# Kernel optimization log

Hardware: AMD Instinct MI355X
Metric: run time of the kernel (lower is better)

## Reference

```python
import jax, jax.numpy as jnp
import numpy as np

EMBED_DIM = 1024
NUM_HEADS = 16
HEAD_DIM = EMBED_DIM // NUM_HEADS


def setup_inputs() -> dict:
    key = jax.random.key(0)
    ks = jax.random.split(key, 12)
    B, S, E = 2, 2048, EMBED_DIM
    scale = 1.0 / np.sqrt(E)
    inp = {
        "query": jax.random.normal(ks[0], (B, S, E), dtype=jnp.float32),
        "key": jax.random.normal(ks[1], (B, S, E), dtype=jnp.float32),
        "value": jax.random.normal(ks[2], (B, S, E), dtype=jnp.float32),
        "key_padding_mask": jax.random.randint(ks[3], (B, S), 0, 2).astype(bool),
        # Linear params (torch nn.Linear: y = x @ W.T + b)
        "Wq": jax.random.normal(ks[4], (E, E), dtype=jnp.float32) * scale,
        "bq": jnp.zeros((E,), dtype=jnp.float32),
        "Wk": jax.random.normal(ks[5], (E, E), dtype=jnp.float32) * scale,
        "bk": jnp.zeros((E,), dtype=jnp.float32),
        "Wv": jax.random.normal(ks[6], (E, E), dtype=jnp.float32) * scale,
        "bv": jnp.zeros((E,), dtype=jnp.float32),
        "Wo": jax.random.normal(ks[7], (E, E), dtype=jnp.float32) * scale,
        "bo": jnp.zeros((E,), dtype=jnp.float32),
    }
    return inp


def reference(query, key, value, key_padding_mask, Wq, bq, Wk, bk, Wv, bv, Wo, bo):
    B, Sq, E = query.shape
    H, D = NUM_HEADS, HEAD_DIM

    def split_heads(x, W, b):
        y = x @ W.T + b                      # [B, S, E]
        return y.reshape(B, -1, H, D).transpose(0, 2, 1, 3)  # [B, H, S, D]

    q = split_heads(query, Wq, bq)
    k = split_heads(key, Wk, bk)
    v = split_heads(value, Wv, bv)

    scores = jnp.einsum("bhqd,bhkd->bhqk", q, k) / jnp.sqrt(jnp.float32(D))
    scores = jnp.where(key_padding_mask[:, None, None, :], -jnp.inf, scores)
    probs = jax.nn.softmax(scores, axis=-1)  # dropout p=0.0 -> identity
    attn = jnp.einsum("bhqk,bhkd->bhqd", probs, v)
    attn = attn.transpose(0, 2, 1, 3).reshape(B, Sq, E)
    return attn @ Wo.T + bo
```

## Files before the change

### kernel.cpp

```cpp
#include <hip/hip_runtime.h>
#include <hip/hip_bf16.h>

#define BATCH 2
#define SEQ   2048
#define EMBED 1024
#define NHEAD 16
#define HDIM  64

typedef __bf16 bf16x8 __attribute__((ext_vector_type(8)));
typedef float  floatx4 __attribute__((ext_vector_type(4)));

__global__ void mask_flags_bits(const void* qptr, const void* mptr,
                                unsigned long long* mb, int* flags) {
    const unsigned int* w = (const unsigned int*)mptr;
    int all01 = 1, allf = 1;
    for (int i = 0; i < 64; ++i) {
        unsigned int x = w[i];
        if (!(x == 0u || x == 1u)) all01 = 0;
        if (!(x == 0u || x == 0x3F800000u)) allf = 0;
    }
    const int bytemask = (all01 || allf) ? 0 : 1;
    const int i = blockIdx.x * 64 + threadIdx.x;
    int v;
    if (bytemask) v = (((const unsigned char*)mptr)[i] != 0);
    else          v = (((const unsigned int*)mptr)[i] != 0u);
    unsigned long long bal = __ballot(v);
    if (threadIdx.x == 0) mb[blockIdx.x] = bal;
    if (blockIdx.x == 0 && threadIdx.x == 0) {
        const unsigned short* u = (const unsigned short*)qptr;
        int sane = 0;
        for (int k = 0; k < 64; ++k) {
            int e = (u[2 * k] >> 7) & 0xff;
            if (e >= 117 && e <= 137) sane++;
        }
        flags[0] = (sane >= 40) ? 1 : 0;
        flags[1] = bytemask;
    }
}

struct ConvAll { const void* src[7]; void* dst[7]; unsigned n[7]; };

__global__ __launch_bounds__(256) void convert_all(ConvAll a, const int* flags) {
    if (flags[0]) return;
    const int t = blockIdx.y;
    const unsigned n8 = a.n[t] / 8;
    const unsigned stride = gridDim.x * blockDim.x;
    for (unsigned i = blockIdx.x * blockDim.x + threadIdx.x; i < n8; i += stride) {
        const unsigned base = i * 8;
        const float* s = (const float*)a.src[t] + base;
        __hip_bfloat16 tmp[8];
#pragma unroll
        for (int j = 0; j < 8; ++j) tmp[j] = __float2bfloat16(s[j]);
        *(uint4*)((__hip_bfloat16*)a.dst[t] + base) = *(const uint4*)tmp;
    }
}

__device__ __forceinline__ void gload_lds16(const __hip_bfloat16* g, __bf16* l) {
    __builtin_amdgcn_global_load_lds(
        (const __attribute__((address_space(1))) unsigned int*)g,
        (__attribute__((address_space(3))) unsigned int*)l, 16, 0, 0);
}

struct GemmIO {
    const void* Xr; const __hip_bfloat16* Xc;
    const void* Wr; const __hip_bfloat16* Wc;
    const void* br;
    void* Y;
    float osc;
};
struct GemmArgs { GemmIO io[3]; };

__global__ __launch_bounds__(256, 2) void gemm_mfma(
        GemmArgs args, int M, int N, int K, const int* flags, int omode) {
    const GemmIO io = args.io[blockIdx.z];
    const int isbf = flags[0];
    const __hip_bfloat16* Xp = isbf ? (const __hip_bfloat16*)io.Xr : io.Xc;
    const __hip_bfloat16* Wp = isbf ? (const __hip_bfloat16*)io.Wr : io.Wc;
    __shared__ __bf16 Xs[128 * 64];
    __shared__ __bf16 Ws[128 * 64];
    const int lane = threadIdx.x & 63, wv = threadIdx.x >> 6;
    const int wr = wv >> 1, wc = wv & 1;
    const int l = lane & 15, quad = lane >> 4;
    const int row0 = blockIdx.y * 128, col0 = blockIdx.x * 128;

    const int srow = lane >> 3;
    const int schunk = (lane & 7) ^ srow;
    const __hip_bfloat16* xbase = Xp + (size_t)(row0 + srow) * K + schunk * 8;
    const __hip_bfloat16* wbase = Wp + (size_t)(col0 + srow) * K + schunk * 8;

    floatx4 acc[4][4] = {};

    for (int k0 = 0; k0 < K; k0 += 64) {
        __syncthreads();
#pragma unroll
        for (int i = 0; i < 4; ++i) {
            const int instr = wv * 4 + i;
            gload_lds16(xbase + (size_t)instr * 8 * K + k0, &Xs[instr * 512]);
        }
#pragma unroll
        for (int i = 0; i < 4; ++i) {
            const int instr = wv * 4 + i;
            gload_lds16(wbase + (size_t)instr * 8 * K + k0, &Ws[instr * 512]);
        }
        __syncthreads();
#pragma unroll
        for (int kk = 0; kk < 2; ++kk) {
            bf16x8 af[4], bfr[4];
#pragma unroll
            for (int m = 0; m < 4; ++m)
                af[m] = *(const bf16x8*)
                    &Xs[(wr * 64 + m * 16 + l) * 64 + ((kk * 4 + quad) ^ (l & 7)) * 8];
#pragma unroll
            for (int n = 0; n < 4; ++n)
                bfr[n] = *(const bf16x8*)
                    &Ws[(wc * 64 + n * 16 + l) * 64 + ((kk * 4 + quad) ^ (l & 7)) * 8];
#pragma unroll
            for (int m = 0; m < 4; ++m)
#pragma unroll
                for (int n = 0; n < 4; ++n)
                    acc[m][n] = __builtin_amdgcn_mfma_f32_16x16x32_bf16(
                        af[m], bfr[n], acc[m][n], 0, 0, 0);
        }
    }

#pragma unroll
    for (int m = 0; m < 4; ++m) {
#pragma unroll
        for (int n = 0; n < 4; ++n) {
            const int col = col0 + wc * 64 + n * 16 + l;
            const float bv = isbf
                ? __bfloat162float(((const __hip_bfloat16*)io.br)[col])
                : ((const float*)io.br)[col];
#pragma unroll
            for (int r = 0; r < 4; ++r) {
                const int row = row0 + wr * 64 + m * 16 + quad * 4 + r;
                const float v = (acc[m][n][r] + bv) * io.osc;
                if (omode == 0 || isbf)
                    ((__hip_bfloat16*)io.Y)[(size_t)row * N + col] = __float2bfloat16(v);
                else
                    ((float*)io.Y)[(size_t)row * N + col] = v;
            }
        }
    }
}

__global__ __launch_bounds__(256, 2) void gemm_out(
        const __hip_bfloat16* __restrict__ X,
        const void* __restrict__ Wr, const __hip_bfloat16* __restrict__ Wc,
        const void* __restrict__ bias, void* __restrict__ Y,
        const int* flags) {
    const int N = EMBED, K = EMBED;
    const int isbf = flags[0];
    const __hip_bfloat16* Wp = isbf ? (const __hip_bfloat16*)Wr : Wc;
    __shared__ __bf16 Xs[64 * 64];
    __shared__ __bf16 Ws[128 * 64];
    const int lane = threadIdx.x & 63, wv = threadIdx.x >> 6;
    const int wr = wv >> 1, wc = wv & 1;
    const int l = lane & 15, quad = lane >> 4;
    const int row0 = blockIdx.y * 64, col0 = blockIdx.x * 128;

    const int srow = lane >> 3;
    const int schunk = (lane & 7) ^ srow;
    const __hip_bfloat16* xbase = X + (size_t)(row0 + srow) * K + schunk * 8;
    const __hip_bfloat16* wbase = Wp + (size_t)(col0 + srow) * K + schunk * 8;

    floatx4 acc[2][4] = {};

    for (int k0 = 0; k0 < K; k0 += 64) {
        __syncthreads();
#pragma unroll
        for (int i = 0; i < 2; ++i) {
            const int instr = wv * 2 + i;
            gload_lds16(xbase + (size_t)instr * 8 * K + k0, &Xs[instr * 512]);
        }
#pragma unroll
        for (int i = 0; i < 4; ++i) {
            const int instr = wv * 4 + i;
            gload_lds16(wbase + (size_t)instr * 8 * K + k0, &Ws[instr * 512]);
        }
        __syncthreads();
#pragma unroll
        for (int kk = 0; kk < 2; ++kk) {
            bf16x8 af[2], bfr[4];
#pragma unroll
            for (int m = 0; m < 2; ++m)
                af[m] = *(const bf16x8*)
                    &Xs[(wr * 32 + m * 16 + l) * 64 + ((kk * 4 + quad) ^ (l & 7)) * 8];
#pragma unroll
            for (int n = 0; n < 4; ++n)
                bfr[n] = *(const bf16x8*)
                    &Ws[(wc * 64 + n * 16 + l) * 64 + ((kk * 4 + quad) ^ (l & 7)) * 8];
#pragma unroll
            for (int m = 0; m < 2; ++m)
#pragma unroll
                for (int n = 0; n < 4; ++n)
                    acc[m][n] = __builtin_amdgcn_mfma_f32_16x16x32_bf16(
                        af[m], bfr[n], acc[m][n], 0, 0, 0);
        }
    }

#pragma unroll
    for (int m = 0; m < 2; ++m) {
#pragma unroll
        for (int n = 0; n < 4; ++n) {
            const int col = col0 + wc * 64 + n * 16 + l;
            const float bv = isbf
                ? __bfloat162float(((const __hip_bfloat16*)bias)[col])
                : ((const float*)bias)[col];
#pragma unroll
            for (int r = 0; r < 4; ++r) {
                const int row = row0 + wr * 32 + m * 16 + quad * 4 + r;
                const float v = acc[m][n][r] + bv;
                if (isbf)
                    ((__hip_bfloat16*)Y)[(size_t)row * N + col] = __float2bfloat16(v);
                else
                    ((float*)Y)[(size_t)row * N + col] = v;
            }
        }
    }
}

__global__ __launch_bounds__(256) void transpose_v(
        const __hip_bfloat16* __restrict__ Vp, __hip_bfloat16* __restrict__ Vt,
        const unsigned long long* __restrict__ mbits) {
    __shared__ __bf16 Ts[64][72];
    const int bh = blockIdx.x, b = bh >> 4, h = bh & 15;
    const int s0 = blockIdx.y * 64;
    const unsigned long long mw = mbits[b * 32 + blockIdx.y];
    const int t = threadIdx.x;
    const int s = t >> 2, c = t & 3;
#pragma unroll
    for (int half = 0; half < 2; ++half) {
        const int cc = c + half * 4;
        bf16x8 v = *(const bf16x8*)(Vp + (size_t)(b * SEQ + s0 + s) * EMBED +
                                    h * HDIM + cc * 8);
#pragma unroll
        for (int j = 0; j < 8; ++j) Ts[cc * 8 + j][s] = v[j];
    }
    __syncthreads();
    const int d = t >> 2;
#pragma unroll
    for (int half = 0; half < 2; ++half) {
        const int cc = c + half * 4;
        bf16x8 v = *(const bf16x8*)&Ts[d][cc * 8];
#pragma unroll
        for (int j = 0; j < 8; ++j)
            if ((mw >> (cc * 8 + j)) & 1ull) v[j] = (__bf16)0.f;
        *(bf16x8*)(Vt + ((size_t)bh * HDIM + d) * SEQ + s0 + cc * 8) = v;
    }
}

__global__ __launch_bounds__(256) void attn_mfma(
        const __hip_bfloat16* __restrict__ Qb,
        const __hip_bfloat16* __restrict__ Kb,
        const __hip_bfloat16* __restrict__ Vt,
        const unsigned long long* __restrict__ mbits,
        __hip_bfloat16* __restrict__ Ao) {
    const int bh = blockIdx.x, b = bh >> 4, h = bh & 15;
    const int q0 = blockIdx.y * 128;
    const int wv = threadIdx.x >> 6, lane = threadIdx.x & 63;
    const int l = lane & 15, quad = lane >> 4;

    __shared__ __bf16 Ks[2][128 * 64];
    __shared__ __bf16 Vs[2][64 * 128];

    bf16x8 aQ[2][2];
#pragma unroll
    for (int g = 0; g < 2; ++g) {
        const int qrow = q0 + wv * 32 + g * 16 + l;
        const __hip_bfloat16* qp =
            Qb + ((size_t)(b * SEQ + qrow)) * EMBED + h * HDIM + quad * 8;
        aQ[g][0] = *(const bf16x8*)qp;
        aQ[g][1] = *(const bf16x8*)(qp + 32);
    }

    floatx4 O[2][4] = {};
    floatx4 Ol[2] = {};
    const int rho = 8 * (l >> 2) + (l & 3);

    const int ksrow = lane >> 3, kpc = lane & 7;
    const int vsrow = lane >> 4, vpc = lane & 15;

    auto stage = [&](int k0, int buf) {
#pragma unroll
        for (int i = 0; i < 4; ++i) {
            const int row = wv * 32 + i * 8 + ksrow;
            const int sc = kpc ^ ((row & 3) | (((row >> 3) & 1) << 2));
            gload_lds16(Kb + ((size_t)(b * SEQ + k0 + row)) * EMBED + h * HDIM +
                            sc * 8,
                        &Ks[buf][(wv * 32 + i * 8) * 64]);
        }
#pragma unroll
        for (int i = 0; i < 4; ++i) {
            const int row = wv * 16 + i * 4 + vsrow;
            const int sc = vpc ^ (row & 15);
            gload_lds16(Vt + ((size_t)(bh * HDIM + row)) * SEQ + k0 + sc * 8,
                        &Vs[buf][(wv * 16 + i * 4) * 128]);
        }
    };

    stage(0, 0);
    const int NT = SEQ / 128;
    for (int t = 0; t < NT; ++t) {
        __syncthreads();
        if (t + 1 < NT) stage((t + 1) * 128, (t + 1) & 1);
        const int buf = t & 1;
        const int k0 = t * 128;

        const unsigned long long mw0 = mbits[b * 32 + (k0 >> 6)];
        const unsigned long long mw1 = mbits[b * 32 + (k0 >> 6) + 1];

#pragma unroll
        for (int kh2 = 0; kh2 < 2; ++kh2) {
            bf16x8 a0[4], a1[4];
#pragma unroll
            for (int n = 0; n < 4; ++n) {
                const int rr = kh2 * 64 + 32 * (n >> 1) + 4 * (n & 1) + rho;
                const int f = (rr & 3) | (((rr >> 3) & 1) << 2);
                a0[n] = *(const bf16x8*)&Ks[buf][rr * 64 + ((quad) ^ f) * 8];
                a1[n] = *(const bf16x8*)&Ks[buf][rr * 64 + ((quad + 4) ^ f) * 8];
            }
            bf16x8 bv[2][4];
#pragma unroll
            for (int kh = 0; kh < 2; ++kh)
#pragma unroll
                for (int dt = 0; dt < 4; ++dt) {
                    const int c = kh2 * 8 + kh * 4 + quad;
                    bv[kh][dt] = *(const bf16x8*)
                        &Vs[buf][(dt * 16 + l) * 128 + (c ^ l) * 8];
                }
            const unsigned long long mw = kh2 ? mw1 : mw0;
            bf16x8 vm[2];
#pragma unroll
            for (int kh = 0; kh < 2; ++kh)
#pragma unroll
                for (int j = 0; j < 8; ++j) {
                    const int bit = kh * 32 + quad * 8 + j;
                    vm[kh][j] = ((mw >> bit) & 1ull) ? (__bf16)0.f : (__bf16)1.0f;
                }

#pragma unroll
            for (int g = 0; g < 2; ++g) {
                floatx4 S[4];
#pragma unroll
                for (int n = 0; n < 4; ++n) {
                    floatx4 c = {};
                    c = __builtin_amdgcn_mfma_f32_16x16x32_bf16(a0[n], aQ[g][0],
                                                                c, 0, 0, 0);
                    c = __builtin_amdgcn_mfma_f32_16x16x32_bf16(a1[n], aQ[g][1],
                                                                c, 0, 0, 0);
                    S[n] = c;
                }
#pragma unroll
                for (int n = 0; n < 4; ++n)
#pragma unroll
                    for (int r = 0; r < 4; ++r) S[n][r] = exp2f(S[n][r]);
#pragma unroll
                for (int kh = 0; kh < 2; ++kh) {
                    bf16x8 ap;
#pragma unroll
                    for (int j = 0; j < 4; ++j) {
                        ap[j]     = (__bf16)S[2 * kh][j];
                        ap[j + 4] = (__bf16)S[2 * kh + 1][j];
                    }
#pragma unroll
                    for (int dt = 0; dt < 4; ++dt)
                        O[g][dt] = __builtin_amdgcn_mfma_f32_16x16x32_bf16(
                            ap, bv[kh][dt], O[g][dt], 0, 0, 0);
                    Ol[g] = __builtin_amdgcn_mfma_f32_16x16x32_bf16(
                        ap, vm[kh], Ol[g], 0, 0, 0);
                }
            }
        }
    }
#pragma unroll
    for (int g = 0; g < 2; ++g)
#pragma unroll
        for (int r = 0; r < 4; ++r) {
            const float lr = Ol[g][r];
            const float inv = (lr > 0.f) ? (1.f / lr) : 0.f;
            const int row = q0 + wv * 32 + g * 16 + quad * 4 + r;
#pragma unroll
            for (int dt = 0; dt < 4; ++dt)
                Ao[((size_t)(b * SEQ + row)) * EMBED + h * HDIM + dt * 16 + l] =
                    __float2bfloat16(O[g][dt][r] * inv);
        }
}

extern "C" void kernel_launch(void* const* d_in, const int* in_sizes, int n_in,
                              void* d_out, int out_size, void* d_ws, size_t ws_size,
                              hipStream_t stream) {
    const void* query = d_in[0];
    const void* key   = d_in[1];
    const void* value = d_in[2];
    const void* mask  = d_in[3];

    char* ws = (char*)d_ws;
    int* flags = (int*)ws;
    unsigned long long* mbits = (unsigned long long*)(ws + 1024);
    const size_t TEN = (size_t)BATCH * SEQ * EMBED;
    const size_t WEL = (size_t)EMBED * EMBED;
    char* p = ws + 32768;
    __hip_bfloat16* Qc  = (__hip_bfloat16*)p;  p += TEN * 2;
    __hip_bfloat16* Kc  = (__hip_bfloat16*)p;  p += TEN * 2;
    __hip_bfloat16* Vc  = (__hip_bfloat16*)p;  p += TEN * 2;
    __hip_bfloat16* Wqc = (__hip_bfloat16*)p;  p += WEL * 2;
    __hip_bfloat16* Wkc = (__hip_bfloat16*)p;  p += WEL * 2;
    __hip_bfloat16* Wvc = (__hip_bfloat16*)p;  p += WEL * 2;
    __hip_bfloat16* Woc = (__hip_bfloat16*)p;  p += WEL * 2;
    __hip_bfloat16* Qb  = (__hip_bfloat16*)p;  p += TEN * 2;
    __hip_bfloat16* Kb  = (__hip_bfloat16*)p;  p += TEN * 2;
    __hip_bfloat16* Vp  = (__hip_bfloat16*)p;  p += TEN * 2;
    __hip_bfloat16* Ao  = Qc;
    __hip_bfloat16* Vt  = Kc;

    const int M = BATCH * SEQ;
    const float QSCALE = 0.125f * 1.44269504088896f;

    mask_flags_bits<<<M / 64, 64, 0, stream>>>(query, mask, mbits, flags);

    ConvAll ca;
    ca.src[0] = query;    ca.dst[0] = Qc;  ca.n[0] = (unsigned)TEN;
    ca.src[1] = key;      ca.dst[1] = Kc;  ca.n[1] = (unsigned)TEN;
    ca.src[2] = value;    ca.dst[2] = Vc;  ca.n[2] = (unsigned)TEN;
    ca.src[3] = d_in[4];  ca.dst[3] = Wqc; ca.n[3] = (unsigned)WEL;
    ca.src[4] = d_in[6];  ca.dst[4] = Wkc; ca.n[4] = (unsigned)WEL;
    ca.src[5] = d_in[8];  ca.dst[5] = Wvc; ca.n[5] = (unsigned)WEL;
    ca.src[6] = d_in[10]; ca.dst[6] = Woc; ca.n[6] = (unsigned)WEL;
    convert_all<<<dim3(64, 7), 256, 0, stream>>>(ca, flags);

    GemmArgs qkv;
    qkv.io[0] = { query, Qc, d_in[4],  Wqc, d_in[5],  (void*)Qb, QSCALE };
    qkv.io[1] = { key,   Kc, d_in[6],  Wkc, d_in[7],  (void*)Kb, 1.0f };
    qkv.io[2] = { value, Vc, d_in[8],  Wvc, d_in[9],  (void*)Vp, 1.0f };
    gemm_mfma<<<dim3(EMBED / 128, M / 128, 3), 256, 0, stream>>>(
        qkv, M, EMBED, EMBED, flags, 0);

    transpose_v<<<dim3(BATCH * NHEAD, SEQ / 64), 256, 0, stream>>>(Vp, Vt, mbits);

    attn_mfma<<<dim3(BATCH * NHEAD, SEQ / 128), 256, 0, stream>>>(
        Qb, Kb, Vt, mbits, Ao);

    gemm_out<<<dim3(EMBED / 128, M / 64), 256, 0, stream>>>(
        Ao, d_in[10], Woc, d_in[11], d_out, flags);
}
```

Before: 258.7 us.

## Read K/V fragments directly from global memory instead of LDS staging

Removes the double-buffered LDS staging of K and V tiles in the attention kernel, so each wave loads its MFMA operands straight from global memory (through the caches) with no per-tile __syncthreads. The per-key mask is precomputed as a bf16 0/1 vector in the mask kernel and loaded as vectors, replacing the per-element bit extraction. Launch bounds now request 4 blocks per CU for higher occupancy. In exchange, the four waves of a block each fetch the same K/V data separately, and the fragment reads are strided and uncoalesced, so the kernel leans heavily on L1/L2 hit rates.

```diff
diff --git a/kernel.cpp b/kernel.cpp
--- a/kernel.cpp
+++ b/kernel.cpp
@@ -11,7 +11,8 @@
 typedef float  floatx4 __attribute__((ext_vector_type(4)));
 
 __global__ void mask_flags_bits(const void* qptr, const void* mptr,
-                                unsigned long long* mb, int* flags) {
+                                unsigned long long* mb, int* flags,
+                                __hip_bfloat16* mones) {
     const unsigned int* w = (const unsigned int*)mptr;
     int all01 = 1, allf = 1;
     for (int i = 0; i < 64; ++i) {
@@ -26,6 +27,7 @@
     else          v = (((const unsigned int*)mptr)[i] != 0u);
     unsigned long long bal = __ballot(v);
     if (threadIdx.x == 0) mb[blockIdx.x] = bal;
+    mones[i] = __float2bfloat16(v ? 0.f : 1.f);
     if (blockIdx.x == 0 && threadIdx.x == 0) {
         const unsigned short* u = (const unsigned short*)qptr;
         int sane = 0;
@@ -250,19 +252,16 @@
     }
 }
 
-__global__ __launch_bounds__(256) void attn_mfma(
+__global__ __launch_bounds__(256, 4) void attn_mfma(
         const __hip_bfloat16* __restrict__ Qb,
         const __hip_bfloat16* __restrict__ Kb,
         const __hip_bfloat16* __restrict__ Vt,
-        const unsigned long long* __restrict__ mbits,
+        const __hip_bfloat16* __restrict__ mones,
         __hip_bfloat16* __restrict__ Ao) {
     const int bh = blockIdx.x, b = bh >> 4, h = bh & 15;
     const int q0 = blockIdx.y * 128;
     const int wv = threadIdx.x >> 6, lane = threadIdx.x & 63;
     const int l = lane & 15, quad = lane >> 4;
-
-    __shared__ __bf16 Ks[2][128 * 64];
-    __shared__ __bf16 Vs[2][64 * 128];
 
     bf16x8 aQ[2][2];
 #pragma unroll
@@ -278,47 +277,23 @@
     floatx4 Ol[2] = {};
     const int rho = 8 * (l >> 2) + (l & 3);
 
-    const int ksrow = lane >> 3, kpc = lane & 7;
-    const int vsrow = lane >> 4, vpc = lane & 15;
-
-    auto stage = [&](int k0, int buf) {
-#pragma unroll
-        for (int i = 0; i < 4; ++i) {
-            const int row = wv * 32 + i * 8 + ksrow;
-            const int sc = kpc ^ ((row & 3) | (((row >> 3) & 1) << 2));
-            gload_lds16(Kb + ((size_t)(b * SEQ + k0 + row)) * EMBED + h * HDIM +
-                            sc * 8,
-                        &Ks[buf][(wv * 32 + i * 8) * 64]);
-        }
-#pragma unroll
-        for (int i = 0; i < 4; ++i) {
-            const int row = wv * 16 + i * 4 + vsrow;
-            const int sc = vpc ^ (row & 15);
-            gload_lds16(Vt + ((size_t)(bh * HDIM + row)) * SEQ + k0 + sc * 8,
-                        &Vs[buf][(wv * 16 + i * 4) * 128]);
-        }
-    };
-
-    stage(0, 0);
+    const __hip_bfloat16* kbase = Kb + (size_t)b * SEQ * EMBED + h * HDIM;
+    const __hip_bfloat16* vbase = Vt + (size_t)bh * HDIM * SEQ;
+    const __hip_bfloat16* mbase = mones + b * SEQ;
+
     const int NT = SEQ / 128;
     for (int t = 0; t < NT; ++t) {
-        __syncthreads();
-        if (t + 1 < NT) stage((t + 1) * 128, (t + 1) & 1);
-        const int buf = t & 1;
         const int k0 = t * 128;
-
-        const unsigned long long mw0 = mbits[b * 32 + (k0 >> 6)];
-        const unsigned long long mw1 = mbits[b * 32 + (k0 >> 6) + 1];
-
 #pragma unroll
         for (int kh2 = 0; kh2 < 2; ++kh2) {
             bf16x8 a0[4], a1[4];
 #pragma unroll
             for (int n = 0; n < 4; ++n) {
                 const int rr = kh2 * 64 + 32 * (n >> 1) + 4 * (n & 1) + rho;
-                const int f = (rr & 3) | (((rr >> 3) & 1) << 2);
-                a0[n] = *(const bf16x8*)&Ks[buf][rr * 64 + ((quad) ^ f) * 8];
-                a1[n] = *(const bf16x8*)&Ks[buf][rr * 64 + ((quad + 4) ^ f) * 8];
+                const __hip_bfloat16* kp =
+                    kbase + (size_t)(k0 + rr) * EMBED + quad * 8;
+                a0[n] = *(const bf16x8*)kp;
+                a1[n] = *(const bf16x8*)(kp + 32);
             }
             bf16x8 bv[2][4];
 #pragma unroll
@@ -327,17 +302,13 @@
                 for (int dt = 0; dt < 4; ++dt) {
                     const int c = kh2 * 8 + kh * 4 + quad;
                     bv[kh][dt] = *(const bf16x8*)
-                        &Vs[buf][(dt * 16 + l) * 128 + (c ^ l) * 8];
+                        (vbase + (size_t)(dt * 16 + l) * SEQ + k0 + c * 8);
                 }
-            const unsigned long long mw = kh2 ? mw1 : mw0;
             bf16x8 vm[2];
 #pragma unroll
             for (int kh = 0; kh < 2; ++kh)
-#pragma unroll
-                for (int j = 0; j < 8; ++j) {
-                    const int bit = kh * 32 + quad * 8 + j;
-                    vm[kh][j] = ((mw >> bit) & 1ull) ? (__bf16)0.f : (__bf16)1.0f;
-                }
+                vm[kh] = *(const bf16x8*)
+                    (mbase + k0 + kh2 * 64 + kh * 32 + quad * 8);
 
 #pragma unroll
             for (int g = 0; g < 2; ++g) {
@@ -398,6 +369,7 @@
     char* ws = (char*)d_ws;
     int* flags = (int*)ws;
     unsigned long long* mbits = (unsigned long long*)(ws + 1024);
+    __hip_bfloat16* mones = (__hip_bfloat16*)(ws + 2048);
     const size_t TEN = (size_t)BATCH * SEQ * EMBED;
     const size_t WEL = (size_t)EMBED * EMBED;
     char* p = ws + 32768;
@@ -417,7 +389,7 @@
     const int M = BATCH * SEQ;
     const float QSCALE = 0.125f * 1.44269504088896f;
 
-    mask_flags_bits<<<M / 64, 64, 0, stream>>>(query, mask, mbits, flags);
+    mask_flags_bits<<<M / 64, 64, 0, stream>>>(query, mask, mbits, flags, mones);
 
     ConvAll ca;
     ca.src[0] = query;    ca.dst[0] = Qc;  ca.n[0] = (unsigned)TEN;
@@ -439,7 +411,7 @@
     transpose_v<<<dim3(BATCH * NHEAD, SEQ / 64), 256, 0, stream>>>(Vp, Vt, mbits);
 
     attn_mfma<<<dim3(BATCH * NHEAD, SEQ / 128), 256, 0, stream>>>(
-        Qb, Kb, Vt, mbits, Ao);
+        Qb, Kb, Vt, mones, Ao);
 
     gemm_out<<<dim3(EMBED / 128, M / 64), 256, 0, stream>>>(
         Ao, d_in[10], Woc, d_in[11], d_out, flags);
```

Measured after the change: 315.6 us. +22.0%, slower.

## Fuse V transpose and masking into QKV GEMM epilogue, precompute bf16 mask vector

Applied to the files above, without the earlier changes.

The V projection GEMM now writes its output directly in the per-head transposed [B,H,D,S] layout and multiplies each row by a precomputed 0/1 bf16 mask. This removes the separate transpose_v kernel launch along with its extra read and write of V. The attention kernel now loads the mask as bf16x8 vectors from a precomputed array instead of expanding bits in registers. The cost is that the V epilogue does strided 8-byte stores, which coalesce worse than the row-major stores.

```diff
diff --git a/kernel.cpp b/kernel.cpp
--- a/kernel.cpp
+++ b/kernel.cpp
@@ -8,10 +8,12 @@
 #define HDIM  64
 
 typedef __bf16 bf16x8 __attribute__((ext_vector_type(8)));
+typedef __bf16 bf16x4 __attribute__((ext_vector_type(4)));
 typedef float  floatx4 __attribute__((ext_vector_type(4)));
 
 __global__ void mask_flags_bits(const void* qptr, const void* mptr,
-                                unsigned long long* mb, int* flags) {
+                                unsigned long long* mb, int* flags,
+                                __hip_bfloat16* mones) {
     const unsigned int* w = (const unsigned int*)mptr;
     int all01 = 1, allf = 1;
     for (int i = 0; i < 64; ++i) {
@@ -26,6 +28,7 @@
     else          v = (((const unsigned int*)mptr)[i] != 0u);
     unsigned long long bal = __ballot(v);
     if (threadIdx.x == 0) mb[blockIdx.x] = bal;
+    mones[i] = __float2bfloat16(v ? 0.f : 1.f);
     if (blockIdx.x == 0 && threadIdx.x == 0) {
         const unsigned short* u = (const unsigned short*)qptr;
         int sane = 0;
@@ -71,7 +74,8 @@
 struct GemmArgs { GemmIO io[3]; };
 
 __global__ __launch_bounds__(256, 2) void gemm_mfma(
-        GemmArgs args, int M, int N, int K, const int* flags, int omode) {
+        GemmArgs args, int M, int N, int K, const int* flags,
+        const __hip_bfloat16* __restrict__ mones) {
     const GemmIO io = args.io[blockIdx.z];
     const int isbf = flags[0];
     const __hip_bfloat16* Xp = isbf ? (const __hip_bfloat16*)io.Xr : io.Xc;
@@ -123,22 +127,45 @@
         }
     }
 
-#pragma unroll
-    for (int m = 0; m < 4; ++m) {
-#pragma unroll
-        for (int n = 0; n < 4; ++n) {
-            const int col = col0 + wc * 64 + n * 16 + l;
-            const float bv = isbf
-                ? __bfloat162float(((const __hip_bfloat16*)io.br)[col])
-                : ((const float*)io.br)[col];
-#pragma unroll
-            for (int r = 0; r < 4; ++r) {
-                const int row = row0 + wr * 64 + m * 16 + quad * 4 + r;
-                const float v = (acc[m][n][r] + bv) * io.osc;
-                if (omode == 0 || isbf)
+    if (blockIdx.z == 2) {
+#pragma unroll
+        for (int m = 0; m < 4; ++m) {
+            const int rb = row0 + wr * 64 + m * 16 + quad * 4;
+            const int b = rb >> 11, s0 = rb & (SEQ - 1);
+            float mf[4];
+#pragma unroll
+            for (int r = 0; r < 4; ++r)
+                mf[r] = __bfloat162float(mones[rb + r]);
+#pragma unroll
+            for (int n = 0; n < 4; ++n) {
+                const int col = col0 + wc * 64 + n * 16 + l;
+                const int h = col >> 6, d = col & 63;
+                const float bv = isbf
+                    ? __bfloat162float(((const __hip_bfloat16*)io.br)[col])
+                    : ((const float*)io.br)[col];
+                bf16x4 out;
+#pragma unroll
+                for (int r = 0; r < 4; ++r)
+                    out[r] = (__bf16)((acc[m][n][r] + bv) * mf[r]);
+                *(bf16x4*)((__hip_bfloat16*)io.Y +
+                           ((size_t)((b << 4) + h) * HDIM + d) * SEQ + s0) = out;
+            }
+        }
+    } else {
+#pragma unroll
+        for (int m = 0; m < 4; ++m) {
+#pragma unroll
+            for (int n = 0; n < 4; ++n) {
+                const int col = col0 + wc * 64 + n * 16 + l;
+                const float bv = isbf
+                    ? __bfloat162float(((const __hip_bfloat16*)io.br)[col])
+                    : ((const float*)io.br)[col];
+#pragma unroll
+                for (int r = 0; r < 4; ++r) {
+                    const int row = row0 + wr * 64 + m * 16 + quad * 4 + r;
+                    const float v = (acc[m][n][r] + bv) * io.osc;
                     ((__hip_bfloat16*)io.Y)[(size_t)row * N + col] = __float2bfloat16(v);
-                else
-                    ((float*)io.Y)[(size_t)row * N + col] = v;
+                }
             }
         }
     }
@@ -220,41 +247,11 @@
     }
 }
 
-__global__ __launch_bounds__(256) void transpose_v(
-        const __hip_bfloat16* __restrict__ Vp, __hip_bfloat16* __restrict__ Vt,
-        const unsigned long long* __restrict__ mbits) {
-    __shared__ __bf16 Ts[64][72];
-    const int bh = blockIdx.x, b = bh >> 4, h = bh & 15;
-    const int s0 = blockIdx.y * 64;
-    const unsigned long long mw = mbits[b * 32 + blockIdx.y];
-    const int t = threadIdx.x;
-    const int s = t >> 2, c = t & 3;
-#pragma unroll
-    for (int half = 0; half < 2; ++half) {
-        const int cc = c + half * 4;
-        bf16x8 v = *(const bf16x8*)(Vp + (size_t)(b * SEQ + s0 + s) * EMBED +
-                                    h * HDIM + cc * 8);
-#pragma unroll
-        for (int j = 0; j < 8; ++j) Ts[cc * 8 + j][s] = v[j];
-    }
-    __syncthreads();
-    const int d = t >> 2;
-#pragma unroll
-    for (int half = 0; half < 2; ++half) {
-        const int cc = c + half * 4;
-        bf16x8 v = *(const bf16x8*)&Ts[d][cc * 8];
-#pragma unroll
-        for (int j = 0; j < 8; ++j)
-            if ((mw >> (cc * 8 + j)) & 1ull) v[j] = (__bf16)0.f;
-        *(bf16x8*)(Vt + ((size_t)bh * HDIM + d) * SEQ + s0 + cc * 8) = v;
-    }
-}
-
 __global__ __launch_bounds__(256) void attn_mfma(
         const __hip_bfloat16* __restrict__ Qb,
         const __hip_bfloat16* __restrict__ Kb,
         const __hip_bfloat16* __restrict__ Vt,
-        const unsigned long long* __restrict__ mbits,
+        const __hip_bfloat16* __restrict__ mones,
         __hip_bfloat16* __restrict__ Ao) {
     const int bh = blockIdx.x, b = bh >> 4, h = bh & 15;
     const int q0 = blockIdx.y * 128;
@@ -280,6 +277,7 @@
 
     const int ksrow = lane >> 3, kpc = lane & 7;
     const int vsrow = lane >> 4, vpc = lane & 15;
+    const __hip_bfloat16* mbase = mones + b * SEQ;
 
     auto stage = [&](int k0, int buf) {
 #pragma unroll
@@ -307,9 +305,6 @@
         const int buf = t & 1;
         const int k0 = t * 128;
 
-        const unsigned long long mw0 = mbits[b * 32 + (k0 >> 6)];
-        const unsigned long long mw1 = mbits[b * 32 + (k0 >> 6) + 1];
-
 #pragma unroll
         for (int kh2 = 0; kh2 < 2; ++kh2) {
             bf16x8 a0[4], a1[4];
@@ -329,15 +324,11 @@
                     bv[kh][dt] = *(const bf16x8*)
                         &Vs[buf][(dt * 16 + l) * 128 + (c ^ l) * 8];
                 }
-            const unsigned long long mw = kh2 ? mw1 : mw0;
             bf16x8 vm[2];
 #pragma unroll
             for (int kh = 0; kh < 2; ++kh)
-#pragma unroll
-                for (int j = 0; j < 8; ++j) {
-                    const int bit = kh * 32 + quad * 8 + j;
-                    vm[kh][j] = ((mw >> bit) & 1ull) ? (__bf16)0.f : (__bf16)1.0f;
-                }
+                vm[kh] = *(const bf16x8*)
+                    (mbase + k0 + kh2 * 64 + kh * 32 + quad * 8);
 
 #pragma unroll
             for (int g = 0; g < 2; ++g) {
@@ -398,6 +389,7 @@
     char* ws = (char*)d_ws;
     int* flags = (int*)ws;
     unsigned long long* mbits = (unsigned long long*)(ws + 1024);
+    __hip_bfloat16* mones = (__hip_bfloat16*)(ws + 2048);
     const size_t TEN = (size_t)BATCH * SEQ * EMBED;
     const size_t WEL = (size_t)EMBED * EMBED;
     char* p = ws + 32768;
@@ -410,14 +402,13 @@
     __hip_bfloat16* Woc = (__hip_bfloat16*)p;  p += WEL * 2;
     __hip_bfloat16* Qb  = (__hip_bfloat16*)p;  p += TEN * 2;
     __hip_bfloat16* Kb  = (__hip_bfloat16*)p;  p += TEN * 2;
-    __hip_bfloat16* Vp  = (__hip_bfloat16*)p;  p += TEN * 2;
+    __hip_bfloat16* Vt  = (__hip_bfloat16*)p;  p += TEN * 2;
     __hip_bfloat16* Ao  = Qc;
-    __hip_bfloat16* Vt  = Kc;
 
     const int M = BATCH * SEQ;
     const float QSCALE = 0.125f * 1.44269504088896f;
 
-    mask_flags_bits<<<M / 64, 64, 0, stream>>>(query, mask, mbits, flags);
+    mask_flags_bits<<<M / 64, 64, 0, stream>>>(query, mask, mbits, flags, mones);
 
     ConvAll ca;
     ca.src[0] = query;    ca.dst[0] = Qc;  ca.n[0] = (unsigned)TEN;
@@ -432,14 +423,12 @@
     GemmArgs qkv;
     qkv.io[0] = { query, Qc, d_in[4],  Wqc, d_in[5],  (void*)Qb, QSCALE };
     qkv.io[1] = { key,   Kc, d_in[6],  Wkc, d_in[7],  (void*)Kb, 1.0f };
-    qkv.io[2] = { value, Vc, d_in[8],  Wvc, d_in[9],  (void*)Vp, 1.0f };
+    qkv.io[2] = { value, Vc, d_in[8],  Wvc, d_in[9],  (void*)Vt, 1.0f };
     gemm_mfma<<<dim3(EMBED / 128, M / 128, 3), 256, 0, stream>>>(
-        qkv, M, EMBED, EMBED, flags, 0);
-
-    transpose_v<<<dim3(BATCH * NHEAD, SEQ / 64), 256, 0, stream>>>(Vp, Vt, mbits);
+        qkv, M, EMBED, EMBED, flags, mones);
 
     attn_mfma<<<dim3(BATCH * NHEAD, SEQ / 128), 256, 0, stream>>>(
-        Qb, Kb, Vt, mbits, Ao);
+        Qb, Kb, Vt, mones, Ao);
 
     gemm_out<<<dim3(EMBED / 128, M / 64), 256, 0, stream>>>(
         Ao, d_in[10], Woc, d_in[11], d_out, flags);
```

Result: faster. 245.1 us (-5.3%).
